# Kernel optimization log

Measured on AMD Instinct MI355X. Metric: run time of the kernel, lower is better.

## Reference

```python
import jax, jax.numpy as jnp
import numpy as np

B, T, F = 512, 1024, 8
H1, H2 = 70, 21   # '80k' config, bidirectional
D1, D2 = 30, 20


def _u(key, shape, fan):
    s = 1.0 / np.sqrt(fan)
    return jax.random.uniform(key, shape, jnp.float32, -s, s)


def setup_inputs() -> dict:
    key = jax.random.key(0)
    ks = iter(jax.random.split(key, 32))
    inp = {"x": jax.random.normal(next(ks), (B, T, F), jnp.float32)}
    # LSTM layer 1 (input F -> H1), forward and backward directions; torch gate order i,f,g,o
    for d in ("f", "b"):
        inp[f"w_ih1_{d}"] = _u(next(ks), (4 * H1, F), H1)
        inp[f"w_hh1_{d}"] = _u(next(ks), (4 * H1, H1), H1)
        inp[f"b_ih1_{d}"] = _u(next(ks), (4 * H1,), H1)
        inp[f"b_hh1_{d}"] = _u(next(ks), (4 * H1,), H1)
    # LSTM layer 2 (input 2*H1 -> H2)
    for d in ("f", "b"):
        inp[f"w_ih2_{d}"] = _u(next(ks), (4 * H2, 2 * H1), H2)
        inp[f"w_hh2_{d}"] = _u(next(ks), (4 * H2, H2), H2)
        inp[f"b_ih2_{d}"] = _u(next(ks), (4 * H2,), H2)
        inp[f"b_hh2_{d}"] = _u(next(ks), (4 * H2,), H2)
    # Dense head: 2*H2 -> D1 -> D2 -> 1
    inp["d1_w"] = _u(next(ks), (D1, 2 * H2), 2 * H2)
    inp["d1_b"] = _u(next(ks), (D1,), 2 * H2)
    inp["d2_w"] = _u(next(ks), (D2, D1), D1)
    inp["d2_b"] = _u(next(ks), (D2,), D1)
    inp["out_w"] = _u(next(ks), (1, D2), D2)
    inp["out_b"] = _u(next(ks), (1,), D2)
    return inp


def _lstm_dir(x, w_ih, w_hh, b_ih, b_hh, reverse):
    # x: [B, T, Fin]; torch LSTM gate order: i, f, g, o
    if reverse:
        x = x[:, ::-1]
    H = w_hh.shape[1]
    pre = jnp.einsum('btf,gf->btg', x, w_ih) + b_ih + b_hh  # [B, T, 4H]
    pre_t = jnp.moveaxis(pre, 1, 0)                          # [T, B, 4H]

    def step(carry, p):
        h, c = carry
        g = p + h @ w_hh.T
        i, f, gg, o = jnp.split(g, 4, axis=-1)
        c = jax.nn.sigmoid(f) * c + jax.nn.sigmoid(i) * jnp.tanh(gg)
        h = jax.nn.sigmoid(o) * jnp.tanh(c)
        return (h, c), h

    init = (jnp.zeros((x.shape[0], H), x.dtype), jnp.zeros((x.shape[0], H), x.dtype))
    _, hs = jax.lax.scan(step, init, pre_t)
    hs = jnp.moveaxis(hs, 0, 1)  # [B, T, H]
    if reverse:
        hs = hs[:, ::-1]
    return hs


def _bilstm(x, wf, uf, bif, bhf, wb, ub, bib, bhb):
    return jnp.concatenate([
        _lstm_dir(x, wf, uf, bif, bhf, reverse=False),
        _lstm_dir(x, wb, ub, bib, bhb, reverse=True),
    ], axis=-1)


def reference(x,
              w_ih1_f, w_hh1_f, b_ih1_f, b_hh1_f,
              w_ih1_b, w_hh1_b, b_ih1_b, b_hh1_b,
              w_ih2_f, w_hh2_f, b_ih2_f, b_hh2_f,
              w_ih2_b, w_hh2_b, b_ih2_b, b_hh2_b,
              d1_w, d1_b, d2_w, d2_b, out_w, out_b):
    h = _bilstm(x, w_ih1_f, w_hh1_f, b_ih1_f, b_hh1_f,
                w_ih1_b, w_hh1_b, b_ih1_b, b_hh1_b)   # [B, T, 2*H1]
    h = _bilstm(h, w_ih2_f, w_hh2_f, b_ih2_f, b_hh2_f,
                w_ih2_b, w_hh2_b, b_ih2_b, b_hh2_b)   # [B, T, 2*H2]
    h = jax.nn.relu(h @ d1_w.T + d1_b)
    h = jax.nn.relu(h @ d2_w.T + d2_b)
    return h @ out_w.T + out_b                          # [B, T, 1]
```

## Files before the change

### kernel.cpp

```cpp
#include <hip/hip_runtime.h>


typedef _Float16 v2f16 __attribute__((ext_vector_type(2)));
typedef _Float16 v4h   __attribute__((ext_vector_type(4)));
typedef _Float16 v8h   __attribute__((ext_vector_type(8)));
typedef float    f32x4 __attribute__((ext_vector_type(4)));

__device__ __forceinline__ float fdot2(v2f16 a, v2f16 b, float c) {
  return __builtin_amdgcn_fdot2(a, b, c, false);
}
#if __has_builtin(__builtin_amdgcn_rcpf)
__device__ __forceinline__ float rcpf(float x) { return __builtin_amdgcn_rcpf(x); }
#else
__device__ __forceinline__ float rcpf(float x) { return 1.f / x; }
#endif
__device__ __forceinline__ float ex2(float v) {
#if __has_builtin(__builtin_amdgcn_exp2f)
  return __builtin_amdgcn_exp2f(v);
#else
  return __expf(v * 0.6931471805599453f);
#endif
}
__device__ __forceinline__ float dpp_xor1(float v) {
  return __builtin_bit_cast(float,
      __builtin_amdgcn_update_dpp(0, __builtin_bit_cast(int, v),
                                  0xB1 , 0xF, 0xF, true));
}

__device__ __forceinline__ void lds_barrier() {
  asm volatile("s_waitcnt lgkmcnt(0)" ::: "memory");
  __builtin_amdgcn_s_barrier();
  __builtin_amdgcn_sched_barrier(0);
}

#define LOG2E  1.4426950408889634f
#define LOG2E2 2.8853900817779268f

#define O_W1M  0u
#define O_WP2  110592u
#define O_W2M  118656u
#define O_BIAS 177792u
#define O_DATA 178496u

__global__ void pack_kernel(const float* __restrict__ wihf, const float* __restrict__ whhf,
                            const float* __restrict__ wihb, const float* __restrict__ whhb,
                            const float* __restrict__ b1if, const float* __restrict__ b1hf,
                            const float* __restrict__ b1ib, const float* __restrict__ b1hb,
                            const float* __restrict__ wih2f, const float* __restrict__ wih2b,
                            const float* __restrict__ whh2f, const float* __restrict__ whh2b,
                            const float* __restrict__ bif, const float* __restrict__ bhf,
                            const float* __restrict__ bib, const float* __restrict__ bhb,
                            char* __restrict__ ws) {
  _Float16* w1m = (_Float16*)(ws + O_W1M);
  _Float16* wp2 = (_Float16*)(ws + O_WP2);
  _Float16* w2m = (_Float16*)(ws + O_W2M);
  float* biasc = (float*)(ws + O_BIAS);
  int idx = blockIdx.x * 256 + threadIdx.x;
  if (idx < 55296) {
    int d = idx / 27648, rem = idx % 27648, rp = rem / 96, k = rem % 96;
    int u = rp >> 2, g = rp & 3;
    const float* wih = d ? wihb : wihf;
    const float* whh = d ? whhb : whhf;
    const float* bi = d ? b1ib : b1if;
    const float* bh = d ? b1hb : b1hf;
    float v = 0.f;
    if (u < 70) {
      int src = g * 70 + u;
      float scale = (g == 2) ? LOG2E2 : LOG2E;
      if (k < 8) v = wih[src * 8 + k] * scale;
      else if (k < 78) v = whh[src * 70 + (k - 8)] * scale;
      else if (k == 78) v = (bi[src] + bh[src]) * scale;
    }
    w1m[idx] = (_Float16)v;
  } else if (idx < 59328) {
    int j = idx - 55296;
    int d = j / 2016, rem = j % 2016, r = rem / 24, k = rem % 24;
    const float* whh = d ? whh2b : whh2f;
    float scale = (r / 21 == 2) ? LOG2E2 : LOG2E;
    wp2[j] = (_Float16)((k < 21) ? whh[r * 21 + k] * scale : 0.f);
  } else if (idx < 88896) {
    int j = idx - 59328;
    int n = j / 168, k = j % 168;
    float v = 0.f;
    if (n < 168 && k < 140) {
      int d = n / 84, m = n % 84, u = m >> 2, g = m & 3;
      const float* wih = d ? wih2b : wih2f;
      float scale = (g == 2) ? LOG2E2 : LOG2E;
      v = wih[(g * 21 + u) * 140 + k] * scale;
    }
    w2m[j] = (_Float16)v;
  } else if (idx < 89072) {
    int n = idx - 88896;
    float v = 0.f;
    if (n < 168) {
      int d = n / 84, m = n % 84, u = m >> 2, g = m & 3;
      const float* bi = d ? bib : bif;
      const float* bh = d ? bhb : bhf;
      float scale = (g == 2) ? LOG2E2 : LOG2E;
      v = (bi[g * 21 + u] + bh[g * 21 + u]) * scale;
    }
    biasc[n] = v;
  }
}

__global__ __launch_bounds__(1024) void lstm1_kernel(
    const float* __restrict__ x,
    const _Float16* __restrict__ w1m,
    _Float16* __restrict__ h1, int b0, int nb) {
  __shared__ __align__(16) _Float16 km[2][16][104];
  const int tid = threadIdx.x;
  const int w = tid >> 6, lane = tid & 63;
  const int q = lane >> 4, bc = lane & 15;
  const int d = blockIdx.y;
  const int blg = blockIdx.x * 16;
  const int gb0 = b0 + blg;

  for (int i = tid; i < 2 * 16 * 104; i += 1024) ((_Float16*)km)[i] = (_Float16)0.f;

  const bool two = (w < 2);
  const int T0 = two ? 2 * w : 2 + w;

  v8h af[2][3];
#pragma unroll
  for (int kc = 0; kc < 3; ++kc)
    af[0][kc] = *(const v8h*)&w1m[(size_t)(d * 288 + T0 * 16 + bc) * 96 + kc * 32 + q * 8];
  if (two) {
#pragma unroll
    for (int kc = 0; kc < 3; ++kc)
      af[1][kc] = *(const v8h*)&w1m[(size_t)(d * 288 + (T0 + 1) * 16 + bc) * 96 + kc * 32 + q * 8];
  }

  __syncthreads();

  if (tid < 16) {
    km[0][tid][78] = (_Float16)1.f;
    km[1][tid][78] = (_Float16)1.f;
  }
  const bool xlane = (tid >= 960 && tid < 992);
  if (xlane) {
    int b = (tid - 960) >> 1, half = (tid - 960) & 1;
    int t0 = d ? 1023 : 0;
    float4 xv = *(const float4*)&x[((size_t)(gb0 + b) * 1024 + t0) * 8 + half * 4];
    v4h xh; xh[0] = (_Float16)xv.x; xh[1] = (_Float16)xv.y;
    xh[2] = (_Float16)xv.z; xh[3] = (_Float16)xv.w;
    *(v4h*)&km[0][b][half * 4] = xh;
  }
  float c0 = 0.f, c1 = 0.f;
  __syncthreads();

#pragma unroll 1
  for (int s = 0; s < 1024; ++s) {
    const int cur = s & 1, nxt = cur ^ 1;
    float4 xv;
    const bool xl = xlane && (s < 1023);
    if (xl) {
      int tn = d ? (1022 - s) : (s + 1);
      xv = *(const float4*)&x[((size_t)(gb0 + ((tid - 960) >> 1)) * 1024 + tn) * 8 + ((tid - 960) & 1) * 4];
    }
    v8h bf0 = *(const v8h*)&km[cur][bc][q * 8];
    v8h bf1 = *(const v8h*)&km[cur][bc][32 + q * 8];
    v8h bf2 = *(const v8h*)&km[cur][bc][64 + q * 8];
    f32x4 z4 = (f32x4){0.f, 0.f, 0.f, 0.f};
    f32x4 A0 = __builtin_amdgcn_mfma_f32_16x16x32_f16(af[0][0], bf0, z4, 0, 0, 0);
    f32x4 A1 = z4;
    if (two) A1 = __builtin_amdgcn_mfma_f32_16x16x32_f16(af[1][0], bf0, z4, 0, 0, 0);
    A0 = __builtin_amdgcn_mfma_f32_16x16x32_f16(af[0][1], bf1, A0, 0, 0, 0);
    if (two) A1 = __builtin_amdgcn_mfma_f32_16x16x32_f16(af[1][1], bf1, A1, 0, 0, 0);
    A0 = __builtin_amdgcn_mfma_f32_16x16x32_f16(af[0][2], bf2, A0, 0, 0, 0);
    if (two) A1 = __builtin_amdgcn_mfma_f32_16x16x32_f16(af[1][2], bf2, A1, 0, 0, 0);
    const int te = d ? (1023 - s) : s;
    const size_t rowb = ((size_t)te * nb + blg + bc) * 176 + d * 70;

#define GATE(Ai, ci, U)                                                      \
    {                                                                        \
      float ei = ex2(-Ai[0]);                                                \
      float ef = ex2(-Ai[1]);                                                \
      float eg = ex2(-Ai[2]);                                                \
      float eo = ex2(-Ai[3]);                                                \
      float si = rcpf(1.f + ei);                                             \
      float sf = rcpf(1.f + ef);                                             \
      float tg = fmaf(2.f, rcpf(1.f + eg), -1.f);                            \
      float so = rcpf(1.f + eo);                                             \
      ci = fmaf(sf, ci, si * tg);                                            \
      float ec = ex2(ci * -LOG2E2);                                          \
      float hv = so * fmaf(2.f, rcpf(1.f + ec), -1.f);                       \
      if ((U) < 70) {                                                        \
        _Float16 hh = (_Float16)hv;                                          \
        km[nxt][bc][8 + (U)] = hh;                                           \
        h1[rowb + (U)] = hh;                                                 \
      }                                                                      \
    }
    GATE(A0, c0, T0 * 4 + q)
    if (two) GATE(A1, c1, (T0 + 1) * 4 + q)
#undef GATE
    if (xl) {
      v4h xh; xh[0] = (_Float16)xv.x; xh[1] = (_Float16)xv.y;
      xh[2] = (_Float16)xv.z; xh[3] = (_Float16)xv.w;
      *(v4h*)&km[nxt][(tid - 960) >> 1][((tid - 960) & 1) * 4] = xh;
    }
    lds_barrier();
  }
}

__global__ __launch_bounds__(256) void pre2_kernel(
    _Float16* __restrict__ h1, const char* __restrict__ ws) {
  const _Float16* w2m = (const _Float16*)(ws + O_W2M);
  const float* biasc = (const float*)(ws + O_BIAS);
  __shared__ _Float16 Al[64][184];
  __shared__ float Bl[176];
  const int tid = threadIdx.x;
  const int r0 = blockIdx.x * 64;
#pragma unroll
  for (int i = 0; i < 6; ++i) {
    int cid = i * 256 + tid;
    if (cid < 1408) {
      int row = cid / 22, ch = cid % 22;
      *(v8h*)&Al[row][ch * 8] = *(const v8h*)&h1[(size_t)(r0 + row) * 176 + ch * 8];
    }
  }
  if (tid < 176) Bl[tid] = biasc[tid];
  __syncthreads();

  const int wv = tid >> 6, lane = tid & 63;
  const int ml = lane & 15, kq = lane >> 4;
  v8h af[5];
#pragma unroll
  for (int k = 0; k < 4; ++k)
    af[k] = *(const v8h*)&Al[wv * 16 + ml][k * 32 + kq * 8];
  {
    v8h a4 = *(const v8h*)&Al[wv * 16 + ml][128 + kq * 8];
    if (kq >= 2) {
#pragma unroll
      for (int j = 0; j < 8; ++j) a4[j] = (_Float16)0.f;
    } else if (kq == 1) {
#pragma unroll
      for (int j = 4; j < 8; ++j) a4[j] = (_Float16)0.f;
    }
    af[4] = a4;
  }

  const v8h* wg = (const v8h*)w2m;
  f32x4 acc[11];
#pragma unroll
  for (int ct = 0; ct < 11; ++ct) acc[ct] = (f32x4){0.f, 0.f, 0.f, 0.f};

  v8h bc[5], bn[5];
#pragma unroll
  for (int k = 0; k < 5; ++k) bn[k] = wg[(size_t)ml * 21 + k * 4 + kq];
#pragma unroll
  for (int ct = 0; ct < 11; ++ct) {
#pragma unroll
    for (int k = 0; k < 5; ++k) bc[k] = bn[k];
    if (ct < 10) {
#pragma unroll
      for (int k = 0; k < 5; ++k) bn[k] = wg[(size_t)((ct + 1) * 16 + ml) * 21 + k * 4 + kq];
    }
#pragma unroll
    for (int k = 0; k < 5; ++k)
      acc[ct] = __builtin_amdgcn_mfma_f32_16x16x32_f16(af[k], bc[k], acc[ct], 0, 0, 0);
  }
  __syncthreads();
#pragma unroll
  for (int ct = 0; ct < 11; ++ct) {
#pragma unroll
    for (int r = 0; r < 4; ++r) {
      int row = wv * 16 + kq * 4 + r, col = ct * 16 + ml;
      Al[row][col] = (_Float16)(acc[ct][r] + Bl[col]);
    }
  }
  __syncthreads();
#pragma unroll
  for (int i = 0; i < 6; ++i) {
    int cid = i * 256 + tid;
    if (cid < 1408) {
      int row = cid / 22, ch = cid % 22;
      *(v8h*)&h1[(size_t)(r0 + row) * 176 + ch * 8] = *(const v8h*)&Al[row][ch * 8];
    }
  }
}

__global__ __launch_bounds__(64) void lstm2_kernel(
    const _Float16* __restrict__ pre2, const _Float16* __restrict__ wp2,
    _Float16* __restrict__ h2, int nb) {
  __shared__ __align__(16) _Float16 kv[2][32];
  const int lane = threadIdx.x;
  const int bl = blockIdx.x;
  const int d = blockIdx.y;
  const int u = lane >> 1, p = lane & 1;
  const bool active = lane < 42;

  ((_Float16*)kv)[lane] = (_Float16)0.f;

  v2f16 w0[12], w1[12];
  if (active) {
    const v8h* wr0 = (const v8h*)&wp2[(d * 84 + (2 * p) * 21 + u) * 24];
    const v8h* wr1 = (const v8h*)&wp2[(d * 84 + (2 * p + 1) * 21 + u) * 24];
#pragma unroll
    for (int ch = 0; ch < 3; ++ch) {
      v8h a = wr0[ch], b = wr1[ch];
#pragma unroll
      for (int q = 0; q < 4; ++q) {
        v2f16 t0; t0[0] = a[2 * q]; t0[1] = a[2 * q + 1]; w0[ch * 4 + q] = t0;
        v2f16 t1; t1[0] = b[2 * q]; t1[1] = b[2 * q + 1]; w1[ch * 4 + q] = t1;
      }
    }
  }
  const int cp = d * 84 + u * 4 + 2 * p;
  const ptrdiff_t dlt = (ptrdiff_t)(d ? -nb : nb) * 176;
  const _Float16* pp = pre2 + ((size_t)(d ? 1023 : 0) * (size_t)nb + bl) * 176;

  v2f16 pa = *(const v2f16*)(pp + cp);
  v2f16 pb = *(const v2f16*)(pp + dlt + cp);
  v2f16 pc = *(const v2f16*)(pp + 2 * dlt + cp);
  v2f16 pd = *(const v2f16*)(pp + 3 * dlt + cp);
  const _Float16* pf = pp + 4 * dlt;

  float cc = 0.f;
  int s = 0;

#define L2STEP(P)                                                           \
  {                                                                         \
    const int cur = s & 1, nxt = cur ^ 1;                                   \
    float A0v = (float)P[0], A1v = (float)P[1];                             \
    const float4* kp = (const float4*)&kv[cur][0];                          \
    float4 q0 = kp[0], q1 = kp[1], q2 = kp[2];                              \
    float x0 = A0v, x1 = 0.f, x2 = 0.f, x3 = 0.f;                           \
    float z0 = A1v, z1 = 0.f, z2 = 0.f, z3 = 0.f;                           \
    x0 = fdot2(__builtin_bit_cast(v2f16, q0.x), w0[0], x0);                 \
    x1 = fdot2(__builtin_bit_cast(v2f16, q0.y), w0[1], x1);                 \
    x2 = fdot2(__builtin_bit_cast(v2f16, q0.z), w0[2], x2);                 \
    x3 = fdot2(__builtin_bit_cast(v2f16, q0.w), w0[3], x3);                 \
    x0 = fdot2(__builtin_bit_cast(v2f16, q1.x), w0[4], x0);                 \
    x1 = fdot2(__builtin_bit_cast(v2f16, q1.y), w0[5], x1);                 \
    x2 = fdot2(__builtin_bit_cast(v2f16, q1.z), w0[6], x2);                 \
    x3 = fdot2(__builtin_bit_cast(v2f16, q1.w), w0[7], x3);                 \
    x0 = fdot2(__builtin_bit_cast(v2f16, q2.x), w0[8], x0);                 \
    x1 = fdot2(__builtin_bit_cast(v2f16, q2.y), w0[9], x1);                 \
    x2 = fdot2(__builtin_bit_cast(v2f16, q2.z), w0[10], x2);                \
    x3 = fdot2(__builtin_bit_cast(v2f16, q2.w), w0[11], x3);                \
    z0 = fdot2(__builtin_bit_cast(v2f16, q0.x), w1[0], z0);                 \
    z1 = fdot2(__builtin_bit_cast(v2f16, q0.y), w1[1], z1);                 \
    z2 = fdot2(__builtin_bit_cast(v2f16, q0.z), w1[2], z2);                 \
    z3 = fdot2(__builtin_bit_cast(v2f16, q0.w), w1[3], z3);                 \
    z0 = fdot2(__builtin_bit_cast(v2f16, q1.x), w1[4], z0);                 \
    z1 = fdot2(__builtin_bit_cast(v2f16, q1.y), w1[5], z1);                 \
    z2 = fdot2(__builtin_bit_cast(v2f16, q1.z), w1[6], z2);                 \
    z3 = fdot2(__builtin_bit_cast(v2f16, q1.w), w1[7], z3);                 \
    z0 = fdot2(__builtin_bit_cast(v2f16, q2.x), w1[8], z0);                 \
    z1 = fdot2(__builtin_bit_cast(v2f16, q2.y), w1[9], z1);                 \
    z2 = fdot2(__builtin_bit_cast(v2f16, q2.z), w1[10], z2);                \
    z3 = fdot2(__builtin_bit_cast(v2f16, q2.w), w1[11], z3);                \
    float A = (x0 + x1) + (x2 + x3), Bv = (z0 + z1) + (z2 + z3);            \
            \
    float r0v = rcpf(1.f + ex2(-A));                                        \
    float Y0 = p ? fmaf(2.f, r0v, -1.f) : r0v;                              \
    float Y1 = rcpf(1.f + ex2(-Bv));                                        \
    float Zs = dpp_xor1(Y0);                                                \
    float Ws = dpp_xor1(Y1);                                                \
    float ai = p ? Zs : Y0;                                                 \
    float af = p ? Ws : Y1;                                                 \
    float ag = p ? Y0 : Zs;                                                 \
    float ao = p ? Y1 : Ws;                                                 \
    cc = fmaf(af, cc, ai * ag);                                             \
    float tc = fmaf(2.f, rcpf(1.f + ex2(cc * -LOG2E2)), -1.f);              \
    float hv = ao * tc;                                                     \
    if (active && p == 0) {                                                 \
      _Float16 hh = (_Float16)hv;                                           \
      int te = d ? (1023 - s) : s;                                          \
      kv[nxt][u] = hh;                                                      \
      h2[((size_t)te * nb + bl) * 48 + d * 21 + u] = hh;                    \
    }                                                                       \
    if (s < 1020) P = *(const v2f16*)(pf + cp);                             \
    pf += dlt;                                                              \
    ++s;                                                                    \
  }

#pragma unroll 1
  for (int it = 0; it < 256; ++it) {
    L2STEP(pa)
    L2STEP(pb)
    L2STEP(pc)
    L2STEP(pd)
  }
#undef L2STEP
}

__global__ __launch_bounds__(256) void head_kernel(
    const _Float16* __restrict__ h2,
    const float* __restrict__ d1w, const float* __restrict__ d1b,
    const float* __restrict__ d2w, const float* __restrict__ d2b,
    const float* __restrict__ ow, const float* __restrict__ ob,
    float* __restrict__ out, int b0, int lognb) {
  int n = blockIdx.x * 256 + threadIdx.x;
  int t = n >> lognb, bl = n & ((1 << lognb) - 1);
  const v8h* hp = (const v8h*)&h2[(size_t)n * 48];
  float in[48];
#pragma unroll
  for (int i = 0; i < 6; ++i) {
    v8h hc = hp[i];
#pragma unroll
    for (int j = 0; j < 8; ++j) in[i * 8 + j] = (float)hc[j];
  }
  float a1[30];
#pragma unroll
  for (int cc = 0; cc < 30; ++cc) {
    float a = d1b[cc];
#pragma unroll
    for (int k = 0; k < 42; ++k) a += in[k] * d1w[cc * 42 + k];
    a1[cc] = fmaxf(a, 0.f);
  }
  float a2[20];
#pragma unroll
  for (int cc = 0; cc < 20; ++cc) {
    float a = d2b[cc];
#pragma unroll
    for (int k = 0; k < 30; ++k) a += a1[k] * d2w[cc * 30 + k];
    a2[cc] = fmaxf(a, 0.f);
  }
  float o = ob[0];
#pragma unroll
  for (int k = 0; k < 20; ++k) o += a2[k] * ow[k];
  out[(size_t)(b0 + bl) * 1024 + t] = o;
}

extern "C" void kernel_launch(void* const* d_in, const int* in_sizes, int n_in,
                              void* d_out, int out_size, void* d_ws, size_t ws_size,
                              hipStream_t stream) {
  const float* x = (const float*)d_in[0];
  const float* wih1f = (const float*)d_in[1];
  const float* whh1f = (const float*)d_in[2];
  const float* bih1f = (const float*)d_in[3];
  const float* bhh1f = (const float*)d_in[4];
  const float* wih1b = (const float*)d_in[5];
  const float* whh1b = (const float*)d_in[6];
  const float* bih1b = (const float*)d_in[7];
  const float* bhh1b = (const float*)d_in[8];
  const float* wih2f = (const float*)d_in[9];
  const float* whh2f = (const float*)d_in[10];
  const float* bih2f = (const float*)d_in[11];
  const float* bhh2f = (const float*)d_in[12];
  const float* wih2b = (const float*)d_in[13];
  const float* whh2b = (const float*)d_in[14];
  const float* bih2b = (const float*)d_in[15];
  const float* bhh2b = (const float*)d_in[16];
  const float* d1w = (const float*)d_in[17];
  const float* d1b = (const float*)d_in[18];
  const float* d2w = (const float*)d_in[19];
  const float* d2b = (const float*)d_in[20];
  const float* ow = (const float*)d_in[21];
  const float* ob = (const float*)d_in[22];
  float* out = (float*)d_out;
  char* wsb = (char*)d_ws;

  const int cands[6] = {1, 2, 4, 8, 16, 32};
  int nslice = 32;
  for (int i = 0; i < 6; ++i) {
    size_t rows = (size_t)(512 / cands[i]) * 1024;
    if (O_DATA + rows * 448 <= ws_size) { nslice = cands[i]; break; }
  }
  const int nb = 512 / nslice;
  int lognb = 0; while ((1 << lognb) < nb) ++lognb;
  const size_t rows = (size_t)nb * 1024;

  _Float16* w1m = (_Float16*)(wsb + O_W1M);
  _Float16* wp2 = (_Float16*)(wsb + O_WP2);
  _Float16* h1  = (_Float16*)(wsb + O_DATA);
  _Float16* h2  = (_Float16*)(wsb + O_DATA + rows * 352);

  pack_kernel<<<348, 256, 0, stream>>>(wih1f, whh1f, wih1b, whh1b,
                                       bih1f, bhh1f, bih1b, bhh1b,
                                       wih2f, wih2b, whh2f, whh2b,
                                       bih2f, bhh2f, bih2b, bhh2b, wsb);

  for (int s = 0; s < nslice; ++s) {
    const int b0 = s * nb;
    lstm1_kernel<<<dim3(nb / 16, 2), 1024, 0, stream>>>(x, w1m, h1, b0, nb);
    pre2_kernel<<<nb * 16, 256, 0, stream>>>(h1, wsb);
    lstm2_kernel<<<dim3(nb, 2), 64, 0, stream>>>(h1, wp2, h2, nb);
    head_kernel<<<nb * 4, 256, 0, stream>>>(h2, d1w, d1b, d2w, d2b, ow, ob,
                                            out, b0, lognb);
  }
}
```

Measured before the change: 1.329 ms.

## Pack eight LSTM2 sequences per block and merge gate reciprocals in LSTM1

```diff
diff --git a/kernel.cpp b/kernel.cpp
--- a/kernel.cpp
+++ b/kernel.cpp
@@ -177,13 +177,12 @@
       float ef = ex2(-Ai[1]);                                                \
       float eg = ex2(-Ai[2]);                                                \
       float eo = ex2(-Ai[3]);                                                \
-      float si = rcpf(1.f + ei);                                             \
       float sf = rcpf(1.f + ef);                                             \
-      float tg = fmaf(2.f, rcpf(1.f + eg), -1.f);                            \
-      float so = rcpf(1.f + eo);                                             \
-      ci = fmaf(sf, ci, si * tg);                                            \
-      float ec = ex2(ci * -LOG2E2);                                          \
-      float hv = so * fmaf(2.f, rcpf(1.f + ec), -1.f);                       \
+      float ig = (1.f - eg) * rcpf((1.f + ei) * (1.f + eg));                 \
+      ci = fmaf(sf, ci, ig);                                                 \
+      float cl = fminf(fmaxf(ci, -14.f), 14.f);                              \
+      float ec = ex2(cl * -LOG2E2);                                          \
+      float hv = (1.f - ec) * rcpf((1.f + eo) * (1.f + ec));                 \
       if ((U) < 70) {                                                        \
         _Float16 hh = (_Float16)hv;                                          \
         km[nxt][bc][8 + (U)] = hh;                                           \
@@ -279,17 +278,20 @@
   }
 }
 
-__global__ __launch_bounds__(64) void lstm2_kernel(
+__global__ __launch_bounds__(512) void lstm2_kernel(
     const _Float16* __restrict__ pre2, const _Float16* __restrict__ wp2,
     _Float16* __restrict__ h2, int nb) {
-  __shared__ __align__(16) _Float16 kv[2][32];
-  const int lane = threadIdx.x;
-  const int bl = blockIdx.x;
-  const int d = blockIdx.y;
+  __shared__ __align__(16) _Float16 kv[8][2][32];
+  const int tid = threadIdx.x;
+  const int w8 = tid >> 6, lane = tid & 63;
+  const int P = blockIdx.x * 8 + w8;
+  if (P >= 2 * nb) return;
+  const int bl = P >> 1, d = P & 1;
   const int u = lane >> 1, p = lane & 1;
   const bool active = lane < 42;
 
-  ((_Float16*)kv)[lane] = (_Float16)0.f;
+  _Float16 (*kvw)[32] = kv[w8];
+  ((_Float16*)kvw)[lane] = (_Float16)0.f;
 
   v2f16 w0[12], w1[12];
   if (active) {
@@ -318,11 +320,11 @@
   float cc = 0.f;
   int s = 0;
 
-#define L2STEP(P)                                                           \
+#define L2STEP(P2)                                                          \
   {                                                                         \
     const int cur = s & 1, nxt = cur ^ 1;                                   \
-    float A0v = (float)P[0], A1v = (float)P[1];                             \
-    const float4* kp = (const float4*)&kv[cur][0];                          \
+    float A0v = (float)P2[0], A1v = (float)P2[1];                           \
+    const float4* kp = (const float4*)&kvw[cur][0];                         \
     float4 q0 = kp[0], q1 = kp[1], q2 = kp[2];                              \
     float x0 = A0v, x1 = 0.f, x2 = 0.f, x3 = 0.f;                           \
     float z0 = A1v, z1 = 0.f, z2 = 0.f, z3 = 0.f;                           \
@@ -367,10 +369,10 @@
     if (active && p == 0) {                                                 \
       _Float16 hh = (_Float16)hv;                                           \
       int te = d ? (1023 - s) : s;                                          \
-      kv[nxt][u] = hh;                                                      \
+      kvw[nxt][u] = hh;                                                     \
       h2[((size_t)te * nb + bl) * 48 + d * 21 + u] = hh;                    \
     }                                                                       \
-    if (s < 1020) P = *(const v2f16*)(pf + cp);                             \
+    if (s < 1020) P2 = *(const v2f16*)(pf + cp);                            \
     pf += dlt;                                                              \
     ++s;                                                                    \
   }
@@ -476,7 +478,7 @@
     const int b0 = s * nb;
     lstm1_kernel<<<dim3(nb / 16, 2), 1024, 0, stream>>>(x, w1m, h1, b0, nb);
     pre2_kernel<<<nb * 16, 256, 0, stream>>>(h1, wsb);
-    lstm2_kernel<<<dim3(nb, 2), 64, 0, stream>>>(h1, wp2, h2, nb);
+    lstm2_kernel<<<(2 * nb + 7) / 8, 512, 0, stream>>>(h1, wp2, h2, nb);
     head_kernel<<<nb * 4, 256, 0, stream>>>(h2, d1w, d1b, d2w, d2b, ow, ob,
                                             out, b0, lognb);
   }
```

Result: slower. 1.357 ms (+2.1%).

## Prefetch x four steps ahead and cut reciprocals in layer-1 LSTM gate math

Applied to the files above, without the earlier changes.

```diff
diff --git a/kernel.cpp b/kernel.cpp
--- a/kernel.cpp
+++ b/kernel.cpp
@@ -137,39 +137,26 @@
     km[1][tid][78] = (_Float16)1.f;
   }
   const bool xlane = (tid >= 960 && tid < 992);
+  const int xb = (tid - 960) >> 1, xhalf = (tid - 960) & 1;
+  float4 xa, xb4, xc, xd;
+  const float* xp = nullptr;
+  const ptrdiff_t xstep = d ? -8 : 8;
   if (xlane) {
-    int b = (tid - 960) >> 1, half = (tid - 960) & 1;
+    const float* xrow = &x[((size_t)(gb0 + xb) * 1024) * 8 + xhalf * 4];
     int t0 = d ? 1023 : 0;
-    float4 xv = *(const float4*)&x[((size_t)(gb0 + b) * 1024 + t0) * 8 + half * 4];
+    float4 xv = *(const float4*)&xrow[(size_t)t0 * 8];
     v4h xh; xh[0] = (_Float16)xv.x; xh[1] = (_Float16)xv.y;
     xh[2] = (_Float16)xv.z; xh[3] = (_Float16)xv.w;
-    *(v4h*)&km[0][b][half * 4] = xh;
+    *(v4h*)&km[0][xb][xhalf * 4] = xh;
+    xa  = *(const float4*)&xrow[(size_t)(d ? 1022 : 1) * 8];
+    xb4 = *(const float4*)&xrow[(size_t)(d ? 1021 : 2) * 8];
+    xc  = *(const float4*)&xrow[(size_t)(d ? 1020 : 3) * 8];
+    xd  = *(const float4*)&xrow[(size_t)(d ? 1019 : 4) * 8];
+    xp  = &xrow[(size_t)(d ? 1018 : 5) * 8];
   }
   float c0 = 0.f, c1 = 0.f;
+  int s = 0;
   __syncthreads();
-
-#pragma unroll 1
-  for (int s = 0; s < 1024; ++s) {
-    const int cur = s & 1, nxt = cur ^ 1;
-    float4 xv;
-    const bool xl = xlane && (s < 1023);
-    if (xl) {
-      int tn = d ? (1022 - s) : (s + 1);
-      xv = *(const float4*)&x[((size_t)(gb0 + ((tid - 960) >> 1)) * 1024 + tn) * 8 + ((tid - 960) & 1) * 4];
-    }
-    v8h bf0 = *(const v8h*)&km[cur][bc][q * 8];
-    v8h bf1 = *(const v8h*)&km[cur][bc][32 + q * 8];
-    v8h bf2 = *(const v8h*)&km[cur][bc][64 + q * 8];
-    f32x4 z4 = (f32x4){0.f, 0.f, 0.f, 0.f};
-    f32x4 A0 = __builtin_amdgcn_mfma_f32_16x16x32_f16(af[0][0], bf0, z4, 0, 0, 0);
-    f32x4 A1 = z4;
-    if (two) A1 = __builtin_amdgcn_mfma_f32_16x16x32_f16(af[1][0], bf0, z4, 0, 0, 0);
-    A0 = __builtin_amdgcn_mfma_f32_16x16x32_f16(af[0][1], bf1, A0, 0, 0, 0);
-    if (two) A1 = __builtin_amdgcn_mfma_f32_16x16x32_f16(af[1][1], bf1, A1, 0, 0, 0);
-    A0 = __builtin_amdgcn_mfma_f32_16x16x32_f16(af[0][2], bf2, A0, 0, 0, 0);
-    if (two) A1 = __builtin_amdgcn_mfma_f32_16x16x32_f16(af[1][2], bf2, A1, 0, 0, 0);
-    const int te = d ? (1023 - s) : s;
-    const size_t rowb = ((size_t)te * nb + blg + bc) * 176 + d * 70;
 
 #define GATE(Ai, ci, U)                                                      \
     {                                                                        \
@@ -177,29 +164,59 @@
       float ef = ex2(-Ai[1]);                                                \
       float eg = ex2(-Ai[2]);                                                \
       float eo = ex2(-Ai[3]);                                                \
-      float si = rcpf(1.f + ei);                                             \
       float sf = rcpf(1.f + ef);                                             \
-      float tg = fmaf(2.f, rcpf(1.f + eg), -1.f);                            \
-      float so = rcpf(1.f + eo);                                             \
-      ci = fmaf(sf, ci, si * tg);                                            \
-      float ec = ex2(ci * -LOG2E2);                                          \
-      float hv = so * fmaf(2.f, rcpf(1.f + ec), -1.f);                       \
+      float ig = (1.f - eg) * rcpf((1.f + ei) * (1.f + eg));                 \
+      ci = fmaf(sf, ci, ig);                                                 \
+      float cl = fminf(fmaxf(ci, -14.f), 14.f);                              \
+      float ec = ex2(cl * -LOG2E2);                                          \
+      float hv = (1.f - ec) * rcpf((1.f + eo) * (1.f + ec));                 \
       if ((U) < 70) {                                                        \
         _Float16 hh = (_Float16)hv;                                          \
         km[nxt][bc][8 + (U)] = hh;                                           \
         h1[rowb + (U)] = hh;                                                 \
       }                                                                      \
     }
-    GATE(A0, c0, T0 * 4 + q)
-    if (two) GATE(A1, c1, (T0 + 1) * 4 + q)
+
+#define STEP1(XR)                                                            \
+  {                                                                          \
+    const int cur = s & 1, nxt = cur ^ 1;                                    \
+    v8h bf0 = *(const v8h*)&km[cur][bc][q * 8];                              \
+    v8h bf1 = *(const v8h*)&km[cur][bc][32 + q * 8];                         \
+    v8h bf2 = *(const v8h*)&km[cur][bc][64 + q * 8];                         \
+    f32x4 z4 = (f32x4){0.f, 0.f, 0.f, 0.f};                                  \
+    f32x4 A0 = __builtin_amdgcn_mfma_f32_16x16x32_f16(af[0][0], bf0, z4, 0, 0, 0); \
+    f32x4 A1 = z4;                                                           \
+    if (two) A1 = __builtin_amdgcn_mfma_f32_16x16x32_f16(af[1][0], bf0, z4, 0, 0, 0); \
+    A0 = __builtin_amdgcn_mfma_f32_16x16x32_f16(af[0][1], bf1, A0, 0, 0, 0); \
+    if (two) A1 = __builtin_amdgcn_mfma_f32_16x16x32_f16(af[1][1], bf1, A1, 0, 0, 0); \
+    A0 = __builtin_amdgcn_mfma_f32_16x16x32_f16(af[0][2], bf2, A0, 0, 0, 0); \
+    if (two) A1 = __builtin_amdgcn_mfma_f32_16x16x32_f16(af[1][2], bf2, A1, 0, 0, 0); \
+    const int te = d ? (1023 - s) : s;                                       \
+    const size_t rowb = ((size_t)te * nb + blg + bc) * 176 + d * 70;         \
+    GATE(A0, c0, T0 * 4 + q)                                                 \
+    if (two) GATE(A1, c1, (T0 + 1) * 4 + q)                                  \
+    if (xlane) {                                                             \
+      if (s < 1023) {                                                        \
+        v4h xh; xh[0] = (_Float16)XR.x; xh[1] = (_Float16)XR.y;              \
+        xh[2] = (_Float16)XR.z; xh[3] = (_Float16)XR.w;                      \
+        *(v4h*)&km[nxt][xb][xhalf * 4] = xh;                                 \
+      }                                                                      \
+      if (s <= 1018) XR = *(const float4*)xp;                                \
+      xp += xstep;                                                           \
+    }                                                                        \
+    ++s;                                                                     \
+    lds_barrier();                                                           \
+  }
+
+#pragma unroll 1
+  for (int it = 0; it < 256; ++it) {
+    STEP1(xa)
+    STEP1(xb4)
+    STEP1(xc)
+    STEP1(xd)
+  }
+#undef STEP1
 #undef GATE
-    if (xl) {
-      v4h xh; xh[0] = (_Float16)xv.x; xh[1] = (_Float16)xv.y;
-      xh[2] = (_Float16)xv.z; xh[3] = (_Float16)xv.w;
-      *(v4h*)&km[nxt][(tid - 960) >> 1][((tid - 960) & 1) * 4] = xh;
-    }
-    lds_barrier();
-  }
 }
 
 __global__ __launch_bounds__(256) void pre2_kernel(
```

Measured after the change: 1.485 ms. 11.7% more time.
